# Optimization experiments

Measured on AMD Instinct MI355X. Metric: run time of the kernel, lower is better.

Reference implementation:

```python
import jax, jax.numpy as jnp
import numpy as np

BATCH, SEQ, DMODEL, NSTATE = 4, 2048, 1024, 16


def setup_inputs() -> dict:
    key = jax.random.key(0)
    ks = jax.random.split(key, 6)
    def lin_w(k, out_d, in_d):
        # torch Linear default init scale ~ 1/sqrt(in_d)
        return jax.random.uniform(k, (out_d, in_d), jnp.float32, -1.0, 1.0) / np.sqrt(in_d).astype(np.float32)
    return {
        "x": jax.random.normal(ks[0], (BATCH, SEQ, DMODEL), jnp.float32),
        "W1": lin_w(ks[1], DMODEL, DMODEL), "b1": jnp.zeros((DMODEL,), jnp.float32),
        "W2": lin_w(ks[2], NSTATE, DMODEL), "b2": jnp.zeros((NSTATE,), jnp.float32),
        "W3": lin_w(ks[3], NSTATE, DMODEL), "b3": jnp.zeros((NSTATE,), jnp.float32),
        # A: xavier_uniform over (d_model, state_size)
        "A": jax.random.uniform(ks[4], (DMODEL, NSTATE), jnp.float32, -1.0, 1.0) * np.sqrt(6.0 / (DMODEL + NSTATE)).astype(np.float32),
    }


def reference(x, W1, b1, W2, b2, W3, b3, A):
    # Projections (bld -> bln / bld)
    Bmat = x @ W2.T + b2                      # (b, l, n)
    Cmat = x @ W3.T + b3                      # (b, l, n)
    delta = jax.nn.softplus(x @ W1.T + b1)    # (b, l, d)
    # Original math (flag=0 path):
    #   dB[b,l,d,n] = delta[b,l,d] * B[b,l,n]
    #   dA = exp(einsum('bld,dn->bldn', delta, A))  -- multiplied by a zeros h, so it
    #        contributes nothing to the output (dead math; A receives zero grad).
    #   h  = dA * 0 + x[...,None] * dB
    #   y  = einsum('bln,bldn->bld', C, h)
    # This reduces exactly to: y = x * delta * sum_n(B * C)
    bc = jnp.einsum('bln,bln->bl', Bmat, Cmat)  # (b, l)
    y = x * delta * bc[..., None]               # (b, l, d)
    return y
```

## Files before the change

### kernel.cpp

```cpp
#include <hip/hip_runtime.h>
#include <hip/hip_bf16.h>
#include <cmath>

#define BATCH 4
#define SEQ 2048
#define DM 1024
#define NS 16
#define M_ROWS (BATCH * SEQ)

typedef short bf16x8 __attribute__((ext_vector_type(8)));
typedef short bf16x4 __attribute__((ext_vector_type(4)));
typedef float f32x4 __attribute__((ext_vector_type(4)));

__device__ __forceinline__ short f2bf(float f) {
    union { float f; unsigned u; } a; a.f = f;
    unsigned u = a.u;
    return (short)((u + 0x7fffu + ((u >> 16) & 1u)) >> 16);
}
__device__ __forceinline__ float bf2f(unsigned short s) {
    union { unsigned u; float f; } a; a.u = ((unsigned)s) << 16;
    return a.f;
}

#define LDS_CAST(p) ((__attribute__((address_space(3))) unsigned*)(p))
#define GLB_CAST(p) ((const __attribute__((address_space(1))) unsigned*)(p))

__global__ void __launch_bounds__(256) convert_all(
    const float* __restrict__ x,  const float* __restrict__ W1,
    const float* __restrict__ W2, const float* __restrict__ W3,
    short* __restrict__ xb, short* __restrict__ W1b, short* __restrict__ Wcb)
{
    const int b = blockIdx.x;
    const int t = threadIdx.x;
    const float4* src; bf16x4* dst; int qbase;
    if (b < 2048)      { src = (const float4*)x;  dst = (bf16x4*)xb;  qbase = b * 1024; }
    else if (b < 2304) { src = (const float4*)W1; dst = (bf16x4*)W1b; qbase = (b - 2048) * 1024; }
    else if (b < 2308) { src = (const float4*)W2; dst = (bf16x4*)Wcb; qbase = (b - 2304) * 1024; }
    else               { src = (const float4*)W3; dst = (bf16x4*)(Wcb + NS * DM); qbase = (b - 2308) * 1024; }
    #pragma unroll
    for (int i = 0; i < 4; i++) {
        int q = qbase + i * 256 + t;
        float4 v = src[q];
        bf16x4 s;
        s.x = f2bf(v.x); s.y = f2bf(v.y); s.z = f2bf(v.z); s.w = f2bf(v.w);
        dst[q] = s;
    }
}

__global__ void __launch_bounds__(256) gemm_fused(
    const short* __restrict__ xb, const short* __restrict__ W1b,
    const short* __restrict__ Wcb, const float* __restrict__ b1,
    const float* __restrict__ b2,  const float* __restrict__ b3,
    float* __restrict__ out)
{
    __shared__ short As[128][64];
    __shared__ short Bs[128][64];
    __shared__ short Wcs[32][64];
    __shared__ float bcs[128];

    const int n0 = blockIdx.x * 128;
    const int m0 = blockIdx.y * 128;
    const int t = threadIdx.x;
    const int lane = t & 63;
    const int w = t >> 6;
    const int wm = (w >> 1) * 64;
    const int wn = (w & 1) * 64;
    const int lm = lane & 15;
    const int quad = lane >> 4;

    const int sr  = t >> 3;
    const int sc  = t & 7;
    const int gch = (sc ^ (sr & 7)) * 8;

    const short* pa = xb  + (size_t)(m0 + sr) * DM + gch;
    const short* pb = W1b + (size_t)(n0 + sr) * DM + gch;
    const short* pw = Wcb + (size_t)sr        * DM + gch;

    f32x4 acc[4][4] = {};
    f32x4 abc[2][2] = {};

    #pragma unroll
    for (int kk = 0; kk < 16; kk++) {
        const int ke = kk * 64;
        #pragma unroll
        for (int u = 0; u < 4; u++) {
            __builtin_amdgcn_global_load_lds(GLB_CAST(pa + (size_t)u * 32 * DM + ke),
                LDS_CAST(&As[u * 32 + sr][sc * 8]), 16, 0, 0);
            __builtin_amdgcn_global_load_lds(GLB_CAST(pb + (size_t)u * 32 * DM + ke),
                LDS_CAST(&Bs[u * 32 + sr][sc * 8]), 16, 0, 0);
        }
        __builtin_amdgcn_global_load_lds(GLB_CAST(pw + ke),
            LDS_CAST(&Wcs[sr][sc * 8]), 16, 0, 0);
        __syncthreads();

        #pragma unroll
        for (int ks = 0; ks < 2; ks++) {
            const int cs = ((ks * 4 + quad) ^ (lm & 7)) * 8;
            bf16x8 af[4], bfv[4], wcv[2];
            #pragma unroll
            for (int i = 0; i < 4; i++)
                af[i] = *(const bf16x8*)&As[wm + i * 16 + lm][cs];
            #pragma unroll
            for (int j = 0; j < 4; j++)
                bfv[j] = *(const bf16x8*)&Bs[wn + j * 16 + lm][cs];
            #pragma unroll
            for (int h = 0; h < 2; h++)
                wcv[h] = *(const bf16x8*)&Wcs[h * 16 + lm][cs];

            #pragma unroll
            for (int i = 0; i < 4; i++)
                #pragma unroll
                for (int j = 0; j < 4; j++)
                    acc[i][j] = __builtin_amdgcn_mfma_f32_16x16x32_bf16(
                        af[i], bfv[j], acc[i][j], 0, 0, 0);

            if (w & 1) {
                #pragma unroll
                for (int h = 0; h < 2; h++) {
                    abc[0][h] = __builtin_amdgcn_mfma_f32_16x16x32_bf16(
                        af[2], wcv[h], abc[0][h], 0, 0, 0);
                    abc[1][h] = __builtin_amdgcn_mfma_f32_16x16x32_bf16(
                        af[3], wcv[h], abc[1][h], 0, 0, 0);
                }
            } else {
                #pragma unroll
                for (int h = 0; h < 2; h++) {
                    abc[0][h] = __builtin_amdgcn_mfma_f32_16x16x32_bf16(
                        af[0], wcv[h], abc[0][h], 0, 0, 0);
                    abc[1][h] = __builtin_amdgcn_mfma_f32_16x16x32_bf16(
                        af[1], wcv[h], abc[1][h], 0, 0, 0);
                }
            }
        }
        __syncthreads();
    }

    float bb2 = b2[lm], bb3 = b3[lm];
    #pragma unroll
    for (int i2 = 0; i2 < 2; i2++) {
        #pragma unroll
        for (int r = 0; r < 4; r++) {
            float p = (abc[i2][0][r] + bb2) * (abc[i2][1][r] + bb3);
            p += __shfl_xor(p, 1);
            p += __shfl_xor(p, 2);
            p += __shfl_xor(p, 4);
            p += __shfl_xor(p, 8);
            if (lm == 0) bcs[wm + (w & 1) * 32 + i2 * 16 + quad * 4 + r] = p;
        }
    }
    __syncthreads();

    const unsigned short* xbu = (const unsigned short*)xb;
    float b1v[4];
    #pragma unroll
    for (int j = 0; j < 4; j++) b1v[j] = b1[n0 + wn + j * 16 + lm];

    #pragma unroll
    for (int i = 0; i < 4; i++) {
        #pragma unroll
        for (int r = 0; r < 4; r++) {
            int lrow = wm + i * 16 + quad * 4 + r;
            int gm = m0 + lrow;
            float bcv = bcs[lrow];
            const unsigned short* xrow = xbu + (size_t)gm * DM + n0 + wn + lm;
            float* orow = out + (size_t)gm * DM + n0 + wn + lm;
            #pragma unroll
            for (int j = 0; j < 4; j++) {
                float z = acc[i][j][r] + b1v[j];
                float az = __builtin_fabsf(z);
                float sp = fmaxf(z, 0.f) + __logf(1.f + __expf(-az));
                orow[j * 16] = bf2f(xrow[j * 16]) * sp * bcv;
            }
        }
    }
}

extern "C" void kernel_launch(void* const* d_in, const int* in_sizes, int n_in,
                              void* d_out, int out_size, void* d_ws, size_t ws_size,
                              hipStream_t stream) {
    const float* x  = (const float*)d_in[0];
    const float* W1 = (const float*)d_in[1];
    const float* b1 = (const float*)d_in[2];
    const float* W2 = (const float*)d_in[3];
    const float* b2 = (const float*)d_in[4];
    const float* W3 = (const float*)d_in[5];
    const float* b3 = (const float*)d_in[6];
    float* out = (float*)d_out;

    char* ws = (char*)d_ws;
    short* xb  = (short*)(ws);
    short* W1b = (short*)(ws + (size_t)16 * 1024 * 1024);
    short* Wcb = (short*)(ws + (size_t)18 * 1024 * 1024);

    convert_all<<<2312, 256, 0, stream>>>(x, W1, W2, W3, xb, W1b, Wcb);

    dim3 grid(DM / 128, M_ROWS / 128);
    gemm_fused<<<grid, 256, 0, stream>>>(xb, W1b, Wcb, b1, b2, b3, out);
}
```

Measured before the change: 124.9 us.

## Double-buffer LDS tiles to overlap global loads with MFMA compute

Measured after the change: 128.4 us. +2.9%, slower.

```diff
diff --git a/kernel.cpp b/kernel.cpp
--- a/kernel.cpp
+++ b/kernel.cpp
@@ -53,9 +53,9 @@
     const float* __restrict__ b2,  const float* __restrict__ b3,
     float* __restrict__ out)
 {
-    __shared__ short As[128][64];
-    __shared__ short Bs[128][64];
-    __shared__ short Wcs[32][64];
+    __shared__ short As[2][128][64];
+    __shared__ short Bs[2][128][64];
+    __shared__ short Wcs[2][32][64];
     __shared__ float bcs[128];
 
     const int n0 = blockIdx.x * 128;
@@ -80,18 +80,32 @@
     f32x4 abc[2][2] = {};
 
     #pragma unroll
+    for (int u = 0; u < 4; u++) {
+        __builtin_amdgcn_global_load_lds(GLB_CAST(pa + (size_t)u * 32 * DM),
+            LDS_CAST(&As[0][u * 32 + sr][sc * 8]), 16, 0, 0);
+        __builtin_amdgcn_global_load_lds(GLB_CAST(pb + (size_t)u * 32 * DM),
+            LDS_CAST(&Bs[0][u * 32 + sr][sc * 8]), 16, 0, 0);
+    }
+    __builtin_amdgcn_global_load_lds(GLB_CAST(pw),
+        LDS_CAST(&Wcs[0][sr][sc * 8]), 16, 0, 0);
+    __syncthreads();
+
+    #pragma unroll
     for (int kk = 0; kk < 16; kk++) {
-        const int ke = kk * 64;
-        #pragma unroll
-        for (int u = 0; u < 4; u++) {
-            __builtin_amdgcn_global_load_lds(GLB_CAST(pa + (size_t)u * 32 * DM + ke),
-                LDS_CAST(&As[u * 32 + sr][sc * 8]), 16, 0, 0);
-            __builtin_amdgcn_global_load_lds(GLB_CAST(pb + (size_t)u * 32 * DM + ke),
-                LDS_CAST(&Bs[u * 32 + sr][sc * 8]), 16, 0, 0);
-        }
-        __builtin_amdgcn_global_load_lds(GLB_CAST(pw + ke),
-            LDS_CAST(&Wcs[sr][sc * 8]), 16, 0, 0);
-        __syncthreads();
+        const int p = kk & 1;
+
+        if (kk < 15) {
+            const int ke = (kk + 1) * 64;
+            #pragma unroll
+            for (int u = 0; u < 4; u++) {
+                __builtin_amdgcn_global_load_lds(GLB_CAST(pa + (size_t)u * 32 * DM + ke),
+                    LDS_CAST(&As[1 - p][u * 32 + sr][sc * 8]), 16, 0, 0);
+                __builtin_amdgcn_global_load_lds(GLB_CAST(pb + (size_t)u * 32 * DM + ke),
+                    LDS_CAST(&Bs[1 - p][u * 32 + sr][sc * 8]), 16, 0, 0);
+            }
+            __builtin_amdgcn_global_load_lds(GLB_CAST(pw + ke),
+                LDS_CAST(&Wcs[1 - p][sr][sc * 8]), 16, 0, 0);
+        }
 
         #pragma unroll
         for (int ks = 0; ks < 2; ks++) {
@@ -99,13 +113,13 @@
             bf16x8 af[4], bfv[4], wcv[2];
             #pragma unroll
             for (int i = 0; i < 4; i++)
-                af[i] = *(const bf16x8*)&As[wm + i * 16 + lm][cs];
+                af[i] = *(const bf16x8*)&As[p][wm + i * 16 + lm][cs];
             #pragma unroll
             for (int j = 0; j < 4; j++)
-                bfv[j] = *(const bf16x8*)&Bs[wn + j * 16 + lm][cs];
+                bfv[j] = *(const bf16x8*)&Bs[p][wn + j * 16 + lm][cs];
             #pragma unroll
             for (int h = 0; h < 2; h++)
-                wcv[h] = *(const bf16x8*)&Wcs[h * 16 + lm][cs];
+                wcv[h] = *(const bf16x8*)&Wcs[p][h * 16 + lm][cs];
 
             #pragma unroll
             for (int i = 0; i < 4; i++)
@@ -132,6 +146,7 @@
                 }
             }
         }
+
         __syncthreads();
     }
 
```
